# Optimization experiments

Measured on AMD Instinct MI355X. Metric: run time of the kernel, lower is better.

## Reference

```python
import jax, jax.numpy as jnp
import numpy as np

B, S, D, H, DH, F = 2, 2048, 1024, 16, 64, 4096
EPS = 1e-5


def layernorm(x, gamma, beta):
    mu = jnp.mean(x, axis=-1, keepdims=True)
    var = jnp.mean((x - mu) ** 2, axis=-1, keepdims=True)
    return (x - mu) * jax.lax.rsqrt(var + EPS) * gamma + beta


def setup_inputs() -> dict:
    key = jax.random.key(0)
    ks = jax.random.split(key, 13)
    sc = 0.02
    return {
        "x": jax.random.normal(ks[0], (B, S, D), jnp.float32),
        "W_Q": jax.random.normal(ks[1], (H, DH, D), jnp.float32) * sc,  # per-head [d_head, d_model]
        "W_K": jax.random.normal(ks[2], (H, DH, D), jnp.float32) * sc,
        "W_V": jax.random.normal(ks[3], (H, DH, D), jnp.float32) * sc,
        "W_O": jax.random.normal(ks[4], (H * DH, D), jnp.float32) * sc,
        "W_up": jax.random.normal(ks[5], (D, F), jnp.float32) * sc,
        "b_up": jax.random.normal(ks[6], (F,), jnp.float32) * sc,
        "W_down": jax.random.normal(ks[7], (F, D), jnp.float32) * sc,
        "b_down": jax.random.normal(ks[8], (D,), jnp.float32) * sc,
        "gamma_1": jnp.ones((D,), jnp.float32),
        "beta_1": jnp.zeros((D,), jnp.float32),
        "gamma_2": jnp.ones((D,), jnp.float32),
        "beta_2": jnp.zeros((D,), jnp.float32),
    }


def reference(x, W_Q, W_K, W_V, W_O, W_up, b_up, W_down, b_down, gamma_1, beta_1, gamma_2, beta_2):
    u = layernorm(x, gamma_1, beta_1)
    # per-head projections: input @ W.t() -> [B, H, S, DH]
    Q = jnp.einsum("bsd,hed->bhse", u, W_Q)
    K = jnp.einsum("bsd,hed->bhse", u, W_K)
    V = jnp.einsum("bsd,hed->bhse", u, W_V)
    # Faithful quirk: original does K.reshape(B, DH, S) (raw reshape, NOT transpose)
    K_r = K.reshape(B, H, DH, S)
    scores = jnp.matmul(Q, K_r) / D  # [B,H,S,S]; quirk: scaled by d_model, not sqrt(d_head)
    attn = jax.nn.softmax(scores, axis=-1)
    heads = jnp.matmul(attn, V)  # [B,H,S,DH]
    heads_cat = heads.transpose(0, 2, 1, 3).reshape(B, S, H * DH)  # concat heads on last dim
    z1 = x + heads_cat @ W_O
    v1 = layernorm(z1, gamma_2, beta_2)
    v3 = jax.nn.gelu(v1 @ W_up + b_up, approximate=False)
    z2 = z1 + v3 @ W_down + b_down
    return z2
```

## Files before the change

### kernel.cpp

```cpp
#include <hip/hip_runtime.h>
#include <hip/hip_bf16.h>


typedef __attribute__((ext_vector_type(8))) short short8v;
typedef __attribute__((ext_vector_type(4))) float f32x4;

__device__ __forceinline__ float b2f(unsigned short u) {
    unsigned int x = ((unsigned int)u) << 16;
    float f;
    __builtin_memcpy(&f, &x, 4);
    return f;
}
__device__ __forceinline__ unsigned short f2b(float f) {
    unsigned int x;
    __builtin_memcpy(&x, &f, 4);
    unsigned int r = (x + 0x7FFFu + ((x >> 16) & 1u)) >> 16;
    return (unsigned short)r;
}
__device__ __forceinline__ void gload16(const unsigned short* g, unsigned short* l) {
    __builtin_amdgcn_global_load_lds(
        (const __attribute__((address_space(1))) unsigned int*)g,
        (__attribute__((address_space(3))) unsigned int*)l, 16, 0, 0);
}
__device__ __forceinline__ bool is_f32(const unsigned int* flagp) {
    return *flagp == 0x3F800000u;
}

__global__ __launch_bounds__(256) void cast_qkv_k(const void* __restrict__ s0,
                                                  const void* __restrict__ s1,
                                                  const void* __restrict__ s2,
                                                  unsigned short* __restrict__ dst,
                                                  const unsigned int* __restrict__ flagp) {
    const bool f32 = is_f32(flagp);
    const int seg = blockIdx.x >> 9;
    const int i = ((blockIdx.x & 511) * 256 + threadIdx.x) * 8;
    const void* src = seg == 0 ? s0 : (seg == 1 ? s1 : s2);
    unsigned short* d = dst + (size_t)seg * 1048576 + i;
    if (f32) {
        const float* s = (const float*)src + i;
        float4 a = *(const float4*)s;
        float4 b = *(const float4*)(s + 4);
        union { unsigned short u[8]; int4 v; } o;
        o.u[0] = f2b(a.x); o.u[1] = f2b(a.y); o.u[2] = f2b(a.z); o.u[3] = f2b(a.w);
        o.u[4] = f2b(b.x); o.u[5] = f2b(b.y); o.u[6] = f2b(b.z); o.u[7] = f2b(b.w);
        *(int4*)d = o.v;
    } else {
        *(int4*)d = *(const int4*)((const unsigned short*)src + i);
    }
}

__global__ __launch_bounds__(256) void cast_small_k(const void* __restrict__ s0,
                                                    const void* __restrict__ s1,
                                                    const void* __restrict__ s2,
                                                    const void* __restrict__ s3,
                                                    const void* __restrict__ s4,
                                                    const void* __restrict__ s5,
                                                    unsigned short* __restrict__ dst,
                                                    const unsigned int* __restrict__ flagp) {
    const bool f32 = is_f32(flagp);
    const int seg = blockIdx.x < 2 ? 0 : blockIdx.x - 1;
    const void* srcs[6] = {s0, s1, s2, s3, s4, s5};
    const int offs[6] = {0, 4096, 5120, 6144, 7168, 8192};
    const int lens[6] = {4096, 1024, 1024, 1024, 1024, 1024};
    const int base = (blockIdx.x < 2 ? blockIdx.x * 2048 : 0);
    const int i = base + threadIdx.x * 8;
    if (i >= lens[seg]) return;
    const void* src = srcs[seg];
    unsigned short* d = dst + offs[seg] + i;
    if (f32) {
        const float* s = (const float*)src + i;
        float4 a = *(const float4*)s;
        float4 b = *(const float4*)(s + 4);
        union { unsigned short u[8]; int4 v; } o;
        o.u[0] = f2b(a.x); o.u[1] = f2b(a.y); o.u[2] = f2b(a.z); o.u[3] = f2b(a.w);
        o.u[4] = f2b(b.x); o.u[5] = f2b(b.y); o.u[6] = f2b(b.z); o.u[7] = f2b(b.w);
        *(int4*)d = o.v;
    } else {
        *(int4*)d = *(const int4*)((const unsigned short*)src + i);
    }
}

__global__ __launch_bounds__(256) void castT_k(const void* __restrict__ src,
                                               unsigned short* __restrict__ dst,
                                               int rows, int cols,
                                               const unsigned int* __restrict__ flagp) {
    const bool f32 = is_f32(flagp);
    __shared__ float tile[32][33];
    const int t = threadIdx.x, tx = t & 31, ty = t >> 5;
    const int c0 = blockIdx.x * 32, r0 = blockIdx.y * 32;
#pragma unroll
    for (int i = 0; i < 4; i++) {
        int r = r0 + ty + i * 8;
        float v;
        if (f32) v = ((const float*)src)[(size_t)r * cols + c0 + tx];
        else     v = b2f(((const unsigned short*)src)[(size_t)r * cols + c0 + tx]);
        tile[ty + i * 8][tx] = v;
    }
    __syncthreads();
#pragma unroll
    for (int i = 0; i < 4; i++) {
        int c = c0 + ty + i * 8;
        dst[(size_t)c * rows + r0 + tx] = f2b(tile[tx][ty + i * 8]);
    }
}

__global__ __launch_bounds__(256) void initz_k(float* __restrict__ dst,
                                               const void* __restrict__ src,
                                               const unsigned int* __restrict__ flagp) {
    const int i = (blockIdx.x * 256 + threadIdx.x) * 4;
    if (is_f32(flagp)) {
        *(float4*)(dst + i) = *(const float4*)((const float*)src + i);
    } else {
        uint2 v = *(const uint2*)((const unsigned short*)src + i);
        float4 o;
        o.x = b2f((unsigned short)(v.x & 0xffff));
        o.y = b2f((unsigned short)(v.x >> 16));
        o.z = b2f((unsigned short)(v.y & 0xffff));
        o.w = b2f((unsigned short)(v.y >> 16));
        *(float4*)(dst + i) = o;
    }
}
__global__ __launch_bounds__(256) void fin_k(const float* __restrict__ src,
                                             void* __restrict__ dst,
                                             const unsigned short* __restrict__ bias,
                                             const unsigned int* __restrict__ flagp) {
    const bool f32 = is_f32(flagp);
    const int i = (blockIdx.x * 256 + threadIdx.x) * 4;
    float4 v = *(const float4*)(src + i);
    int c = i & 1023;
    v.x += b2f(bias[c]); v.y += b2f(bias[c + 1]);
    v.z += b2f(bias[c + 2]); v.w += b2f(bias[c + 3]);
    if (f32) {
        *(float4*)((float*)dst + i) = v;
    } else {
        union { unsigned short u[4]; uint2 q; } o;
        o.u[0] = f2b(v.x); o.u[1] = f2b(v.y); o.u[2] = f2b(v.z); o.u[3] = f2b(v.w);
        *(uint2*)((unsigned short*)dst + i) = o.q;
    }
}

template <int MODE>
__global__ __launch_bounds__(256) void ln_k(const void* __restrict__ inp,
                                            unsigned short* __restrict__ outp,
                                            const unsigned short* __restrict__ gamma,
                                            const unsigned short* __restrict__ beta,
                                            const unsigned int* __restrict__ flagp) {
    const int row = blockIdx.x, t = threadIdx.x;
    float xv[4];
    bool f32 = (MODE == 1) ? true : is_f32(flagp);
    if (f32) {
        const float* p = (const float*)inp + (size_t)row * 1024 + t * 4;
        float4 v = *(const float4*)p;
        xv[0] = v.x; xv[1] = v.y; xv[2] = v.z; xv[3] = v.w;
    } else {
        const unsigned short* p = (const unsigned short*)inp + (size_t)row * 1024 + t * 4;
        uint2 v = *(const uint2*)p;
        xv[0] = b2f((unsigned short)(v.x & 0xffff));
        xv[1] = b2f((unsigned short)(v.x >> 16));
        xv[2] = b2f((unsigned short)(v.y & 0xffff));
        xv[3] = b2f((unsigned short)(v.y >> 16));
    }
    float s = xv[0] + xv[1] + xv[2] + xv[3];
    float q = xv[0] * xv[0] + xv[1] * xv[1] + xv[2] * xv[2] + xv[3] * xv[3];
#pragma unroll
    for (int off = 32; off >= 1; off >>= 1) {
        s += __shfl_xor(s, off);
        q += __shfl_xor(q, off);
    }
    __shared__ float ls[8];
    if ((t & 63) == 0) { ls[t >> 6] = s; ls[4 + (t >> 6)] = q; }
    __syncthreads();
    s = ls[0] + ls[1] + ls[2] + ls[3];
    q = ls[4] + ls[5] + ls[6] + ls[7];
    const float mu = s * (1.f / 1024.f);
    const float rs = rsqrtf(q * (1.f / 1024.f) - mu * mu + 1e-5f);
    union { unsigned short u[4]; uint2 v; } o;
#pragma unroll
    for (int i = 0; i < 4; i++) {
        int c = t * 4 + i;
        o.u[i] = f2b((xv[i] - mu) * rs * b2f(gamma[c]) + b2f(beta[c]));
    }
    *(uint2*)(outp + (size_t)row * 1024 + t * 4) = o.v;
}

template <int EPI>
__global__ __launch_bounds__(256) void gemm_k(const unsigned short* __restrict__ A,
                                              const unsigned short* __restrict__ Bm,
                                              unsigned short* __restrict__ C,
                                              unsigned short* __restrict__ C2,
                                              unsigned short* __restrict__ C3,
                                              const unsigned short* __restrict__ bias,
                                              float* __restrict__ outf,
                                              int N, int ldk, int tilesM, int tilesN,
                                              int kLen) {
    __shared__ unsigned short As[128 * 32];
    __shared__ unsigned short Bs[128 * 32];
    const int t = threadIdx.x;
    const int w = t >> 6, lane = t & 63, ln = t & 15, quad = (t & 63) >> 4;
    const int wm = w >> 1, wn = w & 1;
    const int bm = blockIdx.x % tilesM;
    const int bn = (blockIdx.x / tilesM) % tilesN;
    const int kc = blockIdx.x / (tilesM * tilesN);
    const int m0 = bm << 7, n0 = bn << 7;
    const int k0 = kc * kLen;
    f32x4 acc[4][4] = {};

    const int srow = lane >> 2;
    const int scol = (lane & 3) << 3;

    for (int kt = k0; kt < k0 + kLen; kt += 32) {
        __syncthreads();
#pragma unroll
        for (int r = 0; r < 2; r++) {
            const int blk = r * 4 + w;
            const int row = blk * 16 + srow;
            gload16(&A[(size_t)(m0 + row) * ldk + kt + scol], &As[blk * 512]);
            gload16(&Bm[(size_t)(n0 + row) * ldk + kt + scol], &Bs[blk * 512]);
        }
        asm volatile("s_waitcnt vmcnt(0)" ::: "memory");
        __syncthreads();
        short8v af[4], bfv[4];
#pragma unroll
        for (int mi = 0; mi < 4; mi++)
            af[mi] = *(const short8v*)&As[(wm * 64 + mi * 16 + ln) * 32 + quad * 8];
#pragma unroll
        for (int nj = 0; nj < 4; nj++)
            bfv[nj] = *(const short8v*)&Bs[(wn * 64 + nj * 16 + ln) * 32 + quad * 8];
#pragma unroll
        for (int mi = 0; mi < 4; mi++)
#pragma unroll
            for (int nj = 0; nj < 4; nj++)
                acc[mi][nj] = __builtin_amdgcn_mfma_f32_16x16x32_bf16(
                    af[mi], bfv[nj], acc[mi][nj], 0, 0, 0);
    }

#pragma unroll
    for (int mi = 0; mi < 4; mi++) {
#pragma unroll
        for (int nj = 0; nj < 4; nj++) {
#pragma unroll
            for (int r = 0; r < 4; r++) {
                const int m = m0 + wm * 64 + mi * 16 + quad * 4 + r;
                const int n = n0 + wn * 64 + nj * 16 + ln;
                float v = acc[mi][nj][r];
                if (EPI == 4) {
                    float x = v + b2f(bias[n]);
                    C[(size_t)m * N + n] = f2b(0.5f * x * (1.f + erff(x * 0.70710678118654752f)));
                } else if (EPI == 6) {
                    int b = m >> 11, s = m & 2047;
                    int seg = n >> 10, nn = n & 1023, h = nn >> 6, e = nn & 63;
                    if (seg == 0) {
                        C[(size_t)m * 1024 + nn] = f2b(v);
                    } else if (seg == 1) {
                        C2[((size_t)((b * 16 + h) * 2048 + (s & 31) * 64 + e)) * 64 + (s >> 5)] = f2b(v);
                    } else {
                        C3[((size_t)((b * 16 + h) * 64 + e)) * 2048 + s] = f2b(v);
                    }
                } else {
                    unsafeAtomicAdd(&outf[(size_t)m * N + n], v);
                }
            }
        }
    }
}

__global__ __launch_bounds__(512) void attn_k(const unsigned short* __restrict__ Q,
                                              const unsigned short* __restrict__ Kt,
                                              const unsigned short* __restrict__ Vt,
                                              unsigned short* __restrict__ Hd) {
    __shared__ unsigned short Ks[2][2][128 * 32];
    __shared__ unsigned short Vs[2][4][64 * 32];
    __shared__ unsigned short Ps[128 * 132];
    const int t = threadIdx.x;
    const int w = t >> 6, l = t & 63, ln = t & 15, quad = (t & 63) >> 4;
    const int qt = blockIdx.x & 15, bh = blockIdx.x >> 4;
    const int b = bh >> 4, h = bh & 15;
    const int i0 = qt << 7;

    short8v aq[2];
    {
        const unsigned short* qp =
            Q + ((size_t)(b * 2048 + i0 + w * 16 + ln)) * 1024 + h * 64 + quad * 8;
        aq[0] = *(const short8v*)qp;
        aq[1] = *(const short8v*)(qp + 32);
    }

    const int idx0 = w * 2;
    const size_t kbase = (size_t)bh * 2048 * 64;
    const size_t vbase = (size_t)bh * 64 * 2048;

#pragma unroll
    for (int r = 0; r < 2; r++) {
        int idx2 = idx0 + r;
        int ks = idx2 & 1, J = idx2 >> 1;
        gload16(&Kt[kbase + (size_t)(J * 16 + (l >> 2)) * 64 + ks * 32 + (l & 3) * 8],
                &Ks[0][ks][J * 512]);
        int kk = idx2 >> 2, E = (idx2 & 3) * 16;
        gload16(&Vt[vbase + (size_t)(E + (l >> 2)) * 2048 + kk * 32 + (l & 3) * 8],
                &Vs[0][kk][E * 32]);
    }

    f32x4 O[4] = {};
    float l4[4] = {};
    int cur = 0;

    for (int jt = 0; jt < 16; jt++) {
        asm volatile("s_waitcnt vmcnt(0)" ::: "memory");
        __syncthreads();
        if (jt < 15) {
            const int j1 = (jt + 1) << 7;
#pragma unroll
            for (int r = 0; r < 2; r++) {
                int idx2 = idx0 + r;
                int ks = idx2 & 1, J = idx2 >> 1;
                gload16(&Kt[kbase + (size_t)(j1 + J * 16 + (l >> 2)) * 64 + ks * 32 + (l & 3) * 8],
                        &Ks[cur ^ 1][ks][J * 512]);
                int kk = idx2 >> 2, E = (idx2 & 3) * 16;
                gload16(&Vt[vbase + (size_t)(E + (l >> 2)) * 2048 + j1 + kk * 32 + (l & 3) * 8],
                        &Vs[cur ^ 1][kk][E * 32]);
            }
        }

        f32x4 S[8] = {};
#pragma unroll
        for (int ks = 0; ks < 2; ks++) {
#pragma unroll
            for (int nj = 0; nj < 8; nj++) {
                short8v bk = *(const short8v*)&Ks[cur][ks][(nj * 16 + ln) * 32 + quad * 8];
                S[nj] = __builtin_amdgcn_mfma_f32_16x16x32_bf16(aq[ks], bk, S[nj], 0, 0, 0);
            }
        }
#pragma unroll
        for (int nj = 0; nj < 8; nj++)
#pragma unroll
            for (int r = 0; r < 4; r++) {
                float p = __expf(S[nj][r] * 9.765625e-4f);
                l4[r] += p;
                Ps[(w * 16 + quad * 4 + r) * 132 + nj * 16 + ln] = f2b(p);
            }
#pragma unroll
        for (int kk = 0; kk < 4; kk++) {
            short8v ap = *(const short8v*)&Ps[(w * 16 + ln) * 132 + kk * 32 + quad * 8];
#pragma unroll
            for (int ne = 0; ne < 4; ne++) {
                short8v bv = *(const short8v*)&Vs[cur][kk][(ne * 16 + ln) * 32 + quad * 8];
                O[ne] = __builtin_amdgcn_mfma_f32_16x16x32_bf16(ap, bv, O[ne], 0, 0, 0);
            }
        }
        cur ^= 1;
    }

#pragma unroll
    for (int r = 0; r < 4; r++) {
        float s = l4[r];
        s += __shfl_xor(s, 1);
        s += __shfl_xor(s, 2);
        s += __shfl_xor(s, 4);
        s += __shfl_xor(s, 8);
        l4[r] = s;
    }
#pragma unroll
    for (int ne = 0; ne < 4; ne++)
#pragma unroll
        for (int r = 0; r < 4; r++) {
            int i = i0 + w * 16 + quad * 4 + r;
            int e = ne * 16 + ln;
            Hd[((size_t)(b * 2048 + i)) * 1024 + h * 64 + e] = f2b(O[ne][r] / l4[r]);
        }
}

extern "C" void kernel_launch(void* const* d_in, const int* in_sizes, int n_in,
                              void* d_out, int out_size, void* d_ws, size_t ws_size,
                              hipStream_t stream) {
    const unsigned int* flagp = (const unsigned int*)d_in[9];

    unsigned short* p = (unsigned short*)d_ws;
    unsigned short* Wqkv  = p; p += 3145728;
    unsigned short* WOt   = p; p += 1048576;
    unsigned short* Wupt  = p; p += 4194304;
    unsigned short* Wdnt  = p; p += 4194304;
    unsigned short* smallv = p; p += 9216;
    unsigned short* u     = p; p += 4194304;
    unsigned short* Qc    = p; p += 4194304;
    unsigned short* Ktt   = p; p += 4194304;
    unsigned short* Vtt   = p; p += 4194304;
    unsigned short* hd    = p; p += 4194304;
    float*          z1    = (float*)p;
    unsigned short* bupc = smallv;
    unsigned short* bdnc = smallv + 4096;
    unsigned short* g1c  = smallv + 5120;
    unsigned short* be1c = smallv + 6144;
    unsigned short* g2c  = smallv + 7168;
    unsigned short* be2c = smallv + 8192;
    unsigned short* v1   = u;
    unsigned short* v3   = Qc;

    dim3 blk(256);
    cast_qkv_k<<<1536, blk, 0, stream>>>(d_in[1], d_in[2], d_in[3], Wqkv, flagp);
    castT_k<<<dim3(32, 32),  blk, 0, stream>>>(d_in[4], WOt,  1024, 1024, flagp);
    castT_k<<<dim3(128, 32), blk, 0, stream>>>(d_in[5], Wupt, 1024, 4096, flagp);
    castT_k<<<dim3(32, 128), blk, 0, stream>>>(d_in[7], Wdnt, 4096, 1024, flagp);
    cast_small_k<<<7, blk, 0, stream>>>(d_in[6], d_in[8], d_in[9], d_in[10], d_in[11],
                                        d_in[12], smallv, flagp);

    ln_k<0><<<4096, blk, 0, stream>>>(d_in[0], u, g1c, be1c, flagp);
    gemm_k<6><<<768, blk, 0, stream>>>(u, Wqkv, Qc, Ktt, Vtt, nullptr, nullptr,
                                       3072, 1024, 32, 24, 1024);
    attn_k<<<512, dim3(512), 0, stream>>>(Qc, Ktt, Vtt, hd);
    initz_k<<<4096, blk, 0, stream>>>(z1, d_in[0], flagp);
    gemm_k<7><<<512, blk, 0, stream>>>(hd, WOt, nullptr, nullptr, nullptr, nullptr, z1,
                                       1024, 1024, 32, 8, 512);
    ln_k<1><<<4096, blk, 0, stream>>>(z1, v1, g2c, be2c, flagp);
    gemm_k<4><<<1024, blk, 0, stream>>>(v1, Wupt, v3, nullptr, nullptr, bupc, nullptr,
                                        4096, 1024, 32, 32, 1024);
    gemm_k<7><<<512, blk, 0, stream>>>(v3, Wdnt, nullptr, nullptr, nullptr, nullptr, z1,
                                       1024, 4096, 32, 8, 2048);
    fin_k<<<4096, blk, 0, stream>>>(z1, d_out, bdnc, flagp);
}
```

Measured before the change: 484.2 us.

## Keep attention probabilities in registers via transposed QK MFMA and swizzled V tile

Swaps the MFMA operand order so the score tile comes out transposed, which lets each lane pack its exponentiated probabilities directly into a 16x16x16 MFMA operand. This removes the shared-memory P staging buffer and its write/read round trip. The V tile is reorganized into a single XOR-swizzled 64x128 LDS layout to reduce bank conflicts. The row-sum reduction is simplified and launch bounds request 4 blocks per CU. Risks are correctness in the lane/row mapping of the swizzle and the use of the smaller-K MFMA instruction, which needs twice as many issues.

```diff
diff --git a/kernel.cpp b/kernel.cpp
--- a/kernel.cpp
+++ b/kernel.cpp
@@ -3,6 +3,7 @@
 
 
 typedef __attribute__((ext_vector_type(8))) short short8v;
+typedef __attribute__((ext_vector_type(4))) short short4v;
 typedef __attribute__((ext_vector_type(4))) float f32x4;
 
 __device__ __forceinline__ float b2f(unsigned short u) {
@@ -264,13 +265,12 @@
     }
 }
 
-__global__ __launch_bounds__(512) void attn_k(const unsigned short* __restrict__ Q,
-                                              const unsigned short* __restrict__ Kt,
-                                              const unsigned short* __restrict__ Vt,
-                                              unsigned short* __restrict__ Hd) {
+__global__ __launch_bounds__(512, 4) void attn_k(const unsigned short* __restrict__ Q,
+                                                 const unsigned short* __restrict__ Kt,
+                                                 const unsigned short* __restrict__ Vt,
+                                                 unsigned short* __restrict__ Hd) {
     __shared__ unsigned short Ks[2][2][128 * 32];
-    __shared__ unsigned short Vs[2][4][64 * 32];
-    __shared__ unsigned short Ps[128 * 132];
+    __shared__ unsigned short Vs[2][64 * 128];
     const int t = threadIdx.x;
     const int w = t >> 6, l = t & 63, ln = t & 15, quad = (t & 63) >> 4;
     const int qt = blockIdx.x & 15, bh = blockIdx.x >> 4;
@@ -285,39 +285,44 @@
         aq[1] = *(const short8v*)(qp + 32);
     }
 
-    const int idx0 = w * 2;
-    const size_t kbase = (size_t)bh * 2048 * 64;
-    const size_t vbase = (size_t)bh * 64 * 2048;
-
+    const size_t kbase = (size_t)bh * (2048 * 64);
+    const size_t vbase = (size_t)bh * (64 * 2048);
+
+    size_t ksrc[2]; int klds[2];
+    size_t vsrc[2]; int vlds[2];
 #pragma unroll
     for (int r = 0; r < 2; r++) {
-        int idx2 = idx0 + r;
-        int ks = idx2 & 1, J = idx2 >> 1;
-        gload16(&Kt[kbase + (size_t)(J * 16 + (l >> 2)) * 64 + ks * 32 + (l & 3) * 8],
-                &Ks[0][ks][J * 512]);
-        int kk = idx2 >> 2, E = (idx2 & 3) * 16;
-        gload16(&Vt[vbase + (size_t)(E + (l >> 2)) * 2048 + kk * 32 + (l & 3) * 8],
-                &Vs[0][kk][E * 32]);
+        int idx2 = w * 2 + r;
+        int ksp = idx2 & 1, J = idx2 >> 1;
+        ksrc[r] = (size_t)(J * 16 + (l >> 2)) * 64 + ksp * 32 + (l & 3) * 8;
+        klds[r] = ksp * 4096 + J * 512;
+        int c = idx2;
+        int e = c * 4 + (l >> 4), pp = l & 15;
+        int g = (pp & 8) | ((pp & 7) ^ (e & 7));
+        vsrc[r] = (size_t)e * 2048 + g * 8;
+        vlds[r] = c * 512;
+    }
+
+#pragma unroll
+    for (int r = 0; r < 2; r++) {
+        gload16(Kt + kbase + ksrc[r], &Ks[0][0][0] + klds[r]);
+        gload16(Vt + vbase + vsrc[r], &Vs[0][0] + vlds[r]);
     }
 
     f32x4 O[4] = {};
-    float l4[4] = {};
+    float lsum = 0.f;
     int cur = 0;
+    const float sc = 9.765625e-4f;
 
     for (int jt = 0; jt < 16; jt++) {
         asm volatile("s_waitcnt vmcnt(0)" ::: "memory");
         __syncthreads();
         if (jt < 15) {
-            const int j1 = (jt + 1) << 7;
+            const size_t j1 = (size_t)(jt + 1) << 7;
 #pragma unroll
             for (int r = 0; r < 2; r++) {
-                int idx2 = idx0 + r;
-                int ks = idx2 & 1, J = idx2 >> 1;
-                gload16(&Kt[kbase + (size_t)(j1 + J * 16 + (l >> 2)) * 64 + ks * 32 + (l & 3) * 8],
-                        &Ks[cur ^ 1][ks][J * 512]);
-                int kk = idx2 >> 2, E = (idx2 & 3) * 16;
-                gload16(&Vt[vbase + (size_t)(E + (l >> 2)) * 2048 + j1 + kk * 32 + (l & 3) * 8],
-                        &Vs[cur ^ 1][kk][E * 32]);
+                gload16(Kt + kbase + j1 * 64 + ksrc[r], &Ks[cur ^ 1][0][0] + klds[r]);
+                gload16(Vt + vbase + j1 + vsrc[r], &Vs[cur ^ 1][0] + vlds[r]);
             }
         }
 
@@ -327,46 +332,49 @@
 #pragma unroll
             for (int nj = 0; nj < 8; nj++) {
                 short8v bk = *(const short8v*)&Ks[cur][ks][(nj * 16 + ln) * 32 + quad * 8];
-                S[nj] = __builtin_amdgcn_mfma_f32_16x16x32_bf16(aq[ks], bk, S[nj], 0, 0, 0);
+                S[nj] = __builtin_amdgcn_mfma_f32_16x16x32_bf16(bk, aq[ks], S[nj], 0, 0, 0);
             }
         }
-#pragma unroll
-        for (int nj = 0; nj < 8; nj++)
+        short4v pk[8];
+#pragma unroll
+        for (int nj = 0; nj < 8; nj++) {
+            union { unsigned short u[4]; short4v v; } pu;
 #pragma unroll
             for (int r = 0; r < 4; r++) {
-                float p = __expf(S[nj][r] * 9.765625e-4f);
-                l4[r] += p;
-                Ps[(w * 16 + quad * 4 + r) * 132 + nj * 16 + ln] = f2b(p);
+                float p = __expf(S[nj][r] * sc);
+                lsum += p;
+                pu.u[r] = f2b(p);
             }
-#pragma unroll
-        for (int kk = 0; kk < 4; kk++) {
-            short8v ap = *(const short8v*)&Ps[(w * 16 + ln) * 132 + kk * 32 + quad * 8];
+            pk[nj] = pu.v;
+        }
+#pragma unroll
+        for (int nj = 0; nj < 8; nj++) {
+            int g = 2 * nj + (quad >> 1);
+            int pos = (g & 8) | ((g & 7) ^ (ln & 7));
+            int off = pos * 8 + (quad & 1) * 4;
 #pragma unroll
             for (int ne = 0; ne < 4; ne++) {
-                short8v bv = *(const short8v*)&Vs[cur][kk][(ne * 16 + ln) * 32 + quad * 8];
-                O[ne] = __builtin_amdgcn_mfma_f32_16x16x32_bf16(ap, bv, O[ne], 0, 0, 0);
+                short4v bv = *(const short4v*)&Vs[cur][(ne * 16 + ln) * 128 + off];
+                O[ne] = __builtin_amdgcn_mfma_f32_16x16x16bf16_1k(pk[nj], bv, O[ne], 0, 0, 0);
             }
         }
         cur ^= 1;
     }
 
+    lsum += __shfl_xor(lsum, 16);
+    lsum += __shfl_xor(lsum, 32);
+
 #pragma unroll
     for (int r = 0; r < 4; r++) {
-        float s = l4[r];
-        s += __shfl_xor(s, 1);
-        s += __shfl_xor(s, 2);
-        s += __shfl_xor(s, 4);
-        s += __shfl_xor(s, 8);
-        l4[r] = s;
-    }
-#pragma unroll
-    for (int ne = 0; ne < 4; ne++)
-#pragma unroll
-        for (int r = 0; r < 4; r++) {
+        float lr = __shfl(lsum, quad * 4 + r);
+        float inv = 1.f / lr;
+#pragma unroll
+        for (int ne = 0; ne < 4; ne++) {
             int i = i0 + w * 16 + quad * 4 + r;
             int e = ne * 16 + ln;
-            Hd[((size_t)(b * 2048 + i)) * 1024 + h * 64 + e] = f2b(O[ne][r] / l4[r]);
-        }
+            Hd[((size_t)(b * 2048 + i)) * 1024 + h * 64 + e] = f2b(O[ne][r] * inv);
+        }
+    }
 }
 
 extern "C" void kernel_launch(void* const* d_in, const int* in_sizes, int n_in,
```

Result: faster. 470.3 us (-2.9%).
